# Optimization experiments

Hardware: AMD Instinct MI355X
Metric: run time of the kernel (lower is better)

Reference implementation:

```python
import jax, jax.numpy as jnp
import numpy as np

B, N, K, DIM = 256, 256, 16, 128


def setup_inputs() -> dict:
    key = jax.random.key(0)
    ks = jax.random.split(key, 6)
    return {
        "self_vectors": jax.random.normal(ks[0], (B, N, DIM), dtype=jnp.float32),
        "neighbor_vector": jax.random.normal(ks[1], (B, N, K, DIM), dtype=jnp.float32),
        "batch_size": B,
        "masks": jnp.ones((B, N), dtype=jnp.int32),
        "neighbor_weight": jax.random.uniform(ks[2], (B, N, K), dtype=jnp.float32),
        "extra_vector": jax.random.normal(ks[3], (B, N, DIM), dtype=jnp.float32),
        "w_1": jax.random.normal(ks[4], (DIM + 1, DIM), dtype=jnp.float32) * 0.05,
        "w_2": jax.random.normal(ks[5], (DIM, 1), dtype=jnp.float32) * 0.05,
    }


def reference(self_vectors, neighbor_vector, batch_size, masks, neighbor_weight, extra_vector, w_1, w_2):
    # alpha = cat([extra[:, :, None, :] * neighbor, weight[..., None]], -1) @ w_1
    # Split the concat-matmul to avoid materializing the [B,N,K,dim+1] tensor:
    #   (extra * neighbor) @ w_1[:dim]  +  weight[..., None] * w_1[dim]
    gated = extra_vector[:, :, None, :] * neighbor_vector          # [B,N,K,d]
    alpha = jnp.einsum('bnkd,de->bnke', gated, w_1[:-1]) \
        + neighbor_weight[..., None] * w_1[-1]                      # [B,N,K,d]
    alpha = jax.nn.leaky_relu(alpha, negative_slope=0.2)
    alpha = jnp.einsum('bnkd,do->bnko', alpha, w_2)[..., 0]        # [B,N,K]
    alpha = jax.nn.softmax(alpha, axis=-1)                          # over K neighbors
    out = jnp.einsum('bnk,bnkd->bnd', alpha, neighbor_vector)       # weighted sum
    return out
```

## Files before the change

kernel.cpp:

```cpp
#include <hip/hip_runtime.h>
#include <hip/hip_bf16.h>


#define KN 16
#define DIM 128
#define POS_PER_WAVE 8
#define WAVES_PER_BLOCK 4

typedef __bf16 bf16_t;
typedef bf16_t bf16x8 __attribute__((ext_vector_type(8)));
typedef float f32x4 __attribute__((ext_vector_type(4)));

__global__ __launch_bounds__(256) void agg_kernel(
    const float* __restrict__ nb_g,
    const float* __restrict__ wt_g,
    const float* __restrict__ ex_g,
    const float* __restrict__ w1_g,
    const float* __restrict__ w2_g,
    float* __restrict__ out_g,
    int pos_total)
{
    __shared__ bf16x8 bfrag_lds[8 * 4 * 64];
    __shared__ float  bias_lds[DIM];
    __shared__ float  w2_lds[DIM];

    const int t = threadIdx.x;

    #pragma unroll
    for (int f0 = 0; f0 < 8; ++f0) {
        int f = f0 * 256 + t;
        int e0   = f >> 8;
        int ik   = (f >> 6) & 3;
        int lane = f & 63;
        int q = lane >> 4, m = lane & 15;
        bf16x8 v;
        #pragma unroll
        for (int j = 0; j < 8; ++j) {
            int d = ik * 32 + q * 8 + j;
            v[j] = (bf16_t)w1_g[d * DIM + e0 * 16 + m];
        }
        bfrag_lds[f] = v;
    }
    if (t < DIM) {
        bias_lds[t] = w1_g[128 * DIM + t];
        w2_lds[t]   = w2_g[t];
    }
    __syncthreads();

    const int wave = t >> 6;
    const int lane = t & 63;
    const int q = lane >> 4;
    const int m = lane & 15;
    const long wave_global = (long)blockIdx.x * WAVES_PER_BLOCK + wave;

    for (int it = 0; it < POS_PER_WAVE; ++it) {
        const long p = wave_global * POS_PER_WAVE + it;
        if (p >= pos_total) break;
        const float* nb = nb_g + p * (KN * DIM);
        const float* ex = ex_g + p * DIM;
        const float* wt = wt_g + p * KN;

        float wtq[4];
        #pragma unroll
        for (int r = 0; r < 4; ++r) wtq[r] = wt[q * 4 + r];

        f32x4 ex4[8], nb4[8];
        #pragma unroll
        for (int ik = 0; ik < 4; ++ik) {
            int c = ik * 32 + q * 8;
            ex4[ik * 2]     = *(const f32x4*)(ex + c);
            ex4[ik * 2 + 1] = *(const f32x4*)(ex + c + 4);
            nb4[ik * 2]     = *(const f32x4*)(nb + m * DIM + c);
            nb4[ik * 2 + 1] = *(const f32x4*)(nb + m * DIM + c + 4);
        }

        f32x4 acc[8];
        #pragma unroll
        for (int e0 = 0; e0 < 8; ++e0) acc[e0] = (f32x4){0.f, 0.f, 0.f, 0.f};

        #pragma unroll
        for (int ik = 0; ik < 4; ++ik) {
            bf16x8 afrag;
            #pragma unroll
            for (int j = 0; j < 4; ++j) {
                afrag[j]     = (bf16_t)(ex4[ik * 2][j]     * nb4[ik * 2][j]);
                afrag[j + 4] = (bf16_t)(ex4[ik * 2 + 1][j] * nb4[ik * 2 + 1][j]);
            }
            #pragma unroll
            for (int e0 = 0; e0 < 8; ++e0) {
                acc[e0] = __builtin_amdgcn_mfma_f32_16x16x32_bf16(
                    afrag, bfrag_lds[(e0 * 4 + ik) * 64 + lane], acc[e0], 0, 0, 0);
            }
        }

        float z[4] = {0.f, 0.f, 0.f, 0.f};
        #pragma unroll
        for (int e0 = 0; e0 < 8; ++e0) {
            float bias = bias_lds[e0 * 16 + m];
            float w2v  = w2_lds[e0 * 16 + m];
            #pragma unroll
            for (int r = 0; r < 4; ++r) {
                float a = acc[e0][r] + wtq[r] * bias;
                a = fmaxf(a, 0.2f * a);
                z[r] += a * w2v;
            }
        }
        #pragma unroll
        for (int s = 1; s <= 8; s <<= 1) {
            #pragma unroll
            for (int r = 0; r < 4; ++r) z[r] += __shfl_xor(z[r], s, 64);
        }

        float mx = fmaxf(fmaxf(z[0], z[1]), fmaxf(z[2], z[3]));
        mx = fmaxf(mx, __shfl_xor(mx, 16, 64));
        mx = fmaxf(mx, __shfl_xor(mx, 32, 64));
        float e[4], part = 0.f;
        #pragma unroll
        for (int r = 0; r < 4; ++r) { e[r] = __expf(z[r] - mx); part += e[r]; }
        float denom = part;
        denom += __shfl_xor(denom, 16, 64);
        denom += __shfl_xor(denom, 32, 64);
        float inv = 1.f / denom;
        float al[4];
        #pragma unroll
        for (int r = 0; r < 4; ++r) al[r] = e[r] * inv;

        float alpha[16];
        #pragma unroll
        for (int k = 0; k < 16; ++k)
            alpha[k] = __shfl(al[k & 3], (k >> 2) << 4, 64);

        const int d0 = lane * 2;
        float ox = 0.f, oy = 0.f;
        #pragma unroll
        for (int k = 0; k < 16; ++k) {
            float2 v = *(const float2*)(nb + k * DIM + d0);
            ox += alpha[k] * v.x;
            oy += alpha[k] * v.y;
        }
        float2 o = {ox, oy};
        *(float2*)(out_g + p * DIM + d0) = o;
    }
}

extern "C" void kernel_launch(void* const* d_in, const int* in_sizes, int n_in,
                              void* d_out, int out_size, void* d_ws, size_t ws_size,
                              hipStream_t stream) {
    const float* nb = (const float*)d_in[1];
    const float* wt = (const float*)d_in[4];
    const float* ex = (const float*)d_in[5];
    const float* w1 = (const float*)d_in[6];
    const float* w2 = (const float*)d_in[7];
    float* out = (float*)d_out;

    const int pos_total = in_sizes[5] / DIM;
    const int waves = (pos_total + POS_PER_WAVE - 1) / POS_PER_WAVE;
    const int blocks = (waves + WAVES_PER_BLOCK - 1) / WAVES_PER_BLOCK;

    agg_kernel<<<blocks, 256, 0, stream>>>(nb, wt, ex, w1, w2, out, pos_total);
}
```

Before: 756.8 us.

## Unroll per-wave position loop, use DPP reductions, and keep bias/w2 in registers

Moves the per-position work into an inlined helper and fully unrolls the eight positions per wave when no tail exists, so loads for later positions can be scheduled ahead of earlier compute. The row-16 score reduction uses DPP moves instead of shuffles. Each lane rebuilds all 16 softmax scores through xor-shuffles instead of broadcasting alpha, and division by the denominator is deferred to the output. Bias and w2 slices are held in registers rather than LDS. Full unrolling raises register pressure, which could lower occupancy.

```diff
diff --git a/kernel.cpp b/kernel.cpp
--- a/kernel.cpp
+++ b/kernel.cpp
@@ -11,6 +11,117 @@
 typedef bf16_t bf16x8 __attribute__((ext_vector_type(8)));
 typedef float f32x4 __attribute__((ext_vector_type(4)));
 
+template <int CTRL>
+__device__ __forceinline__ float dpp_mov_f32(float x) {
+    return __int_as_float(__builtin_amdgcn_update_dpp(
+        0, __float_as_int(x), CTRL, 0xF, 0xF, true));
+}
+
+__device__ __forceinline__ float row16_sum(float v) {
+    v += dpp_mov_f32<0xB1>(v);
+    v += dpp_mov_f32<0x4E>(v);
+    v += dpp_mov_f32<0x124>(v);
+    v += dpp_mov_f32<0x128>(v);
+    return v;
+}
+
+__device__ __forceinline__ void process_pos(
+    const float* __restrict__ nb,
+    const float* __restrict__ ex,
+    const float* __restrict__ wt,
+    float* __restrict__ outp,
+    const bf16x8* __restrict__ bfrag_lds,
+    const float* __restrict__ bias_r,
+    const float* __restrict__ w2_r,
+    int lane, int q, int m)
+{
+    f32x4 wt4 = *(const f32x4*)(wt + q * 4);
+
+    bf16x8 afrag[4];
+    #pragma unroll
+    for (int ik = 0; ik < 4; ++ik) {
+        const int c = ik * 32 + q * 8;
+        f32x4 ex0 = *(const f32x4*)(ex + c);
+        f32x4 ex1 = *(const f32x4*)(ex + c + 4);
+        f32x4 nb0 = *(const f32x4*)(nb + m * DIM + c);
+        f32x4 nb1 = *(const f32x4*)(nb + m * DIM + c + 4);
+        #pragma unroll
+        for (int j = 0; j < 4; ++j) {
+            afrag[ik][j]     = (bf16_t)(ex0[j] * nb0[j]);
+            afrag[ik][j + 4] = (bf16_t)(ex1[j] * nb1[j]);
+        }
+    }
+
+    f32x4 acc[8];
+    #pragma unroll
+    for (int e0 = 0; e0 < 8; ++e0) acc[e0] = (f32x4){0.f, 0.f, 0.f, 0.f};
+    #pragma unroll
+    for (int e0 = 0; e0 < 8; ++e0) {
+        #pragma unroll
+        for (int ik = 0; ik < 4; ++ik) {
+            acc[e0] = __builtin_amdgcn_mfma_f32_16x16x32_bf16(
+                afrag[ik], bfrag_lds[(e0 * 4 + ik) * 64 + lane], acc[e0],
+                0, 0, 0);
+        }
+    }
+
+    float z[4];
+    #pragma unroll
+    for (int r = 0; r < 4; ++r) {
+        float s = 0.f;
+        #pragma unroll
+        for (int e0 = 0; e0 < 8; ++e0) {
+            float a = acc[e0][r] + wt4[r] * bias_r[e0];
+            a = fmaxf(a, 0.2f * a);
+            s += a * w2_r[e0];
+        }
+        z[r] = row16_sum(s);
+    }
+
+    float zs[4][4];
+    #pragma unroll
+    for (int r = 0; r < 4; ++r) {
+        zs[0][r] = z[r];
+        zs[1][r] = __shfl_xor(z[r], 16, 64);
+    }
+    #pragma unroll
+    for (int r = 0; r < 4; ++r) {
+        zs[2][r] = __shfl_xor(zs[0][r], 32, 64);
+        zs[3][r] = __shfl_xor(zs[1][r], 32, 64);
+    }
+
+    float mx = zs[0][0];
+    #pragma unroll
+    for (int s = 0; s < 4; ++s)
+        #pragma unroll
+        for (int r = 0; r < 4; ++r) mx = fmaxf(mx, zs[s][r]);
+    float al[4][4];
+    float den = 0.f;
+    #pragma unroll
+    for (int s = 0; s < 4; ++s)
+        #pragma unroll
+        for (int r = 0; r < 4; ++r) {
+            al[s][r] = __expf(zs[s][r] - mx);
+            den += al[s][r];
+        }
+    const float inv = 1.f / den;
+
+    const int d0 = lane * 2;
+    float ox = 0.f, oy = 0.f;
+    #pragma unroll
+    for (int s = 0; s < 4; ++s) {
+        const float* nbk = nb + ((q ^ s) * 4) * DIM + d0;
+        #pragma unroll
+        for (int r = 0; r < 4; ++r) {
+            float2 v = *(const float2*)(nbk + r * DIM);
+            ox += al[s][r] * v.x;
+            oy += al[s][r] * v.y;
+        }
+    }
+    float2 o = {ox * inv, oy * inv};
+    *(float2*)(outp + d0) = o;
+}
+
 __global__ __launch_bounds__(256) void agg_kernel(
     const float* __restrict__ nb_g,
     const float* __restrict__ wt_g,
@@ -21,29 +132,22 @@
     int pos_total)
 {
     __shared__ bf16x8 bfrag_lds[8 * 4 * 64];
-    __shared__ float  bias_lds[DIM];
-    __shared__ float  w2_lds[DIM];
 
     const int t = threadIdx.x;
-
     #pragma unroll
     for (int f0 = 0; f0 < 8; ++f0) {
         int f = f0 * 256 + t;
         int e0   = f >> 8;
         int ik   = (f >> 6) & 3;
         int lane = f & 63;
-        int q = lane >> 4, m = lane & 15;
+        int qq = lane >> 4, mm = lane & 15;
         bf16x8 v;
         #pragma unroll
         for (int j = 0; j < 8; ++j) {
-            int d = ik * 32 + q * 8 + j;
-            v[j] = (bf16_t)w1_g[d * DIM + e0 * 16 + m];
+            int d = ik * 32 + qq * 8 + j;
+            v[j] = (bf16_t)w1_g[d * DIM + e0 * 16 + mm];
         }
         bfrag_lds[f] = v;
-    }
-    if (t < DIM) {
-        bias_lds[t] = w1_g[128 * DIM + t];
-        w2_lds[t]   = w2_g[t];
     }
     __syncthreads();
 
@@ -51,95 +155,29 @@
     const int lane = t & 63;
     const int q = lane >> 4;
     const int m = lane & 15;
+
+    float bias_r[8], w2_r[8];
+    #pragma unroll
+    for (int e0 = 0; e0 < 8; ++e0) {
+        bias_r[e0] = w1_g[128 * DIM + e0 * 16 + m];
+        w2_r[e0]   = w2_g[e0 * 16 + m];
+    }
+
     const long wave_global = (long)blockIdx.x * WAVES_PER_BLOCK + wave;
+    const long p0 = wave_global * POS_PER_WAVE;
 
-    for (int it = 0; it < POS_PER_WAVE; ++it) {
-        const long p = wave_global * POS_PER_WAVE + it;
-        if (p >= pos_total) break;
-        const float* nb = nb_g + p * (KN * DIM);
-        const float* ex = ex_g + p * DIM;
-        const float* wt = wt_g + p * KN;
-
-        float wtq[4];
+    if (p0 + POS_PER_WAVE <= pos_total) {
         #pragma unroll
-        for (int r = 0; r < 4; ++r) wtq[r] = wt[q * 4 + r];
-
-        f32x4 ex4[8], nb4[8];
-        #pragma unroll
-        for (int ik = 0; ik < 4; ++ik) {
-            int c = ik * 32 + q * 8;
-            ex4[ik * 2]     = *(const f32x4*)(ex + c);
-            ex4[ik * 2 + 1] = *(const f32x4*)(ex + c + 4);
-            nb4[ik * 2]     = *(const f32x4*)(nb + m * DIM + c);
-            nb4[ik * 2 + 1] = *(const f32x4*)(nb + m * DIM + c + 4);
+        for (int it = 0; it < POS_PER_WAVE; ++it) {
+            const long p = p0 + it;
+            process_pos(nb_g + p * (KN * DIM), ex_g + p * DIM, wt_g + p * KN,
+                        out_g + p * DIM, bfrag_lds, bias_r, w2_r, lane, q, m);
         }
-
-        f32x4 acc[8];
-        #pragma unroll
-        for (int e0 = 0; e0 < 8; ++e0) acc[e0] = (f32x4){0.f, 0.f, 0.f, 0.f};
-
-        #pragma unroll
-        for (int ik = 0; ik < 4; ++ik) {
-            bf16x8 afrag;
-            #pragma unroll
-            for (int j = 0; j < 4; ++j) {
-                afrag[j]     = (bf16_t)(ex4[ik * 2][j]     * nb4[ik * 2][j]);
-                afrag[j + 4] = (bf16_t)(ex4[ik * 2 + 1][j] * nb4[ik * 2 + 1][j]);
-            }
-            #pragma unroll
-            for (int e0 = 0; e0 < 8; ++e0) {
-                acc[e0] = __builtin_amdgcn_mfma_f32_16x16x32_bf16(
-                    afrag, bfrag_lds[(e0 * 4 + ik) * 64 + lane], acc[e0], 0, 0, 0);
-            }
+    } else {
+        for (long p = p0; p < pos_total; ++p) {
+            process_pos(nb_g + p * (KN * DIM), ex_g + p * DIM, wt_g + p * KN,
+                        out_g + p * DIM, bfrag_lds, bias_r, w2_r, lane, q, m);
         }
-
-        float z[4] = {0.f, 0.f, 0.f, 0.f};
-        #pragma unroll
-        for (int e0 = 0; e0 < 8; ++e0) {
-            float bias = bias_lds[e0 * 16 + m];
-            float w2v  = w2_lds[e0 * 16 + m];
-            #pragma unroll
-            for (int r = 0; r < 4; ++r) {
-                float a = acc[e0][r] + wtq[r] * bias;
-                a = fmaxf(a, 0.2f * a);
-                z[r] += a * w2v;
-            }
-        }
-        #pragma unroll
-        for (int s = 1; s <= 8; s <<= 1) {
-            #pragma unroll
-            for (int r = 0; r < 4; ++r) z[r] += __shfl_xor(z[r], s, 64);
-        }
-
-        float mx = fmaxf(fmaxf(z[0], z[1]), fmaxf(z[2], z[3]));
-        mx = fmaxf(mx, __shfl_xor(mx, 16, 64));
-        mx = fmaxf(mx, __shfl_xor(mx, 32, 64));
-        float e[4], part = 0.f;
-        #pragma unroll
-        for (int r = 0; r < 4; ++r) { e[r] = __expf(z[r] - mx); part += e[r]; }
-        float denom = part;
-        denom += __shfl_xor(denom, 16, 64);
-        denom += __shfl_xor(denom, 32, 64);
-        float inv = 1.f / denom;
-        float al[4];
-        #pragma unroll
-        for (int r = 0; r < 4; ++r) al[r] = e[r] * inv;
-
-        float alpha[16];
-        #pragma unroll
-        for (int k = 0; k < 16; ++k)
-            alpha[k] = __shfl(al[k & 3], (k >> 2) << 4, 64);
-
-        const int d0 = lane * 2;
-        float ox = 0.f, oy = 0.f;
-        #pragma unroll
-        for (int k = 0; k < 16; ++k) {
-            float2 v = *(const float2*)(nb + k * DIM + d0);
-            ox += alpha[k] * v.x;
-            oy += alpha[k] * v.y;
-        }
-        float2 o = {ox, oy};
-        *(float2*)(out_g + p * DIM + d0) = o;
     }
 }
 
@@ -154,8 +192,8 @@
     float* out = (float*)d_out;
 
     const int pos_total = in_sizes[5] / DIM;
-    const int waves = (pos_total + POS_PER_WAVE - 1) / POS_PER_WAVE;
-    const int blocks = (waves + WAVES_PER_BLOCK - 1) / WAVES_PER_BLOCK;
+    const long waves = ((long)pos_total + POS_PER_WAVE - 1) / POS_PER_WAVE;
+    const int blocks = (int)((waves + WAVES_PER_BLOCK - 1) / WAVES_PER_BLOCK);
 
     agg_kernel<<<blocks, 256, 0, stream>>>(nb, wt, ex, w1, w2, out, pos_total);
 }
```

Result: slower. 902.7 us (+19.3%).
